# Kernel tuning notes

Hardware: AMD Instinct MI355X
Metric: run time of the kernel (lower is better)

Reference implementation:

```python
import jax, jax.numpy as jnp
import numpy as np

B, T, OBS = 256, 512, 256
H = 128          # OptimizedLSTMCell hidden size (hardcoded in module)
LATENT = 16


def setup_inputs() -> dict:
    key = jax.random.key(0)
    ks = jax.random.split(key, 6)
    xs = jax.random.normal(ks[0], (B, T, OBS), dtype=jnp.float32)
    # fused LSTM weights: gates ordered (i, f, g, o), each of width H
    Wx = jax.random.normal(ks[1], (OBS, 4 * H), dtype=jnp.float32) / np.sqrt(OBS)
    Wh = jax.random.normal(ks[2], (H, 4 * H), dtype=jnp.float32) / np.sqrt(H)
    b = jnp.zeros((4 * H,), dtype=jnp.float32)
    W1 = jax.random.normal(ks[3], (H, H), dtype=jnp.float32) / np.sqrt(H)
    b1 = jnp.zeros((H,), dtype=jnp.float32)
    W2 = jax.random.normal(ks[4], (H, 2 * LATENT), dtype=jnp.float32) / np.sqrt(H)
    b2 = jnp.zeros((2 * LATENT,), dtype=jnp.float32)
    return {"xs": xs, "Wx": Wx, "Wh": Wh, "b": b,
            "W1": W1, "b1": b1, "W2": W2, "b2": b2}


def reference(xs, Wx, Wh, b, W1, b1, W2, b2):
    # LSTM over time (flax OptimizedLSTMCell math, zero initial carry)
    bsz = xs.shape[0]
    hdim = Wh.shape[0]

    def step(carry, x_t):
        c, h = carry
        gates = x_t @ Wx + h @ Wh + b            # [B, 4H]
        i, f, g, o = jnp.split(gates, 4, axis=-1)
        i = jax.nn.sigmoid(i)
        f = jax.nn.sigmoid(f)
        g = jnp.tanh(g)
        o = jax.nn.sigmoid(o)
        c = f * c + i * g
        h = o * jnp.tanh(c)
        return (c, h), None

    init = (jnp.zeros((bsz, hdim), xs.dtype), jnp.zeros((bsz, hdim), xs.dtype))
    (_, h_last), _ = jax.lax.scan(step, init, jnp.swapaxes(xs, 0, 1))

    out = jax.nn.relu(h_last @ W1 + b1)          # [B, H]
    p = out @ W2 + b2                            # [B, 2*latent]
    mean, logvar = jnp.split(p, 2, axis=-1)
    return mean, logvar
```

## Files before the change

kernel.cpp:

```cpp
#include <hip/hip_runtime.h>
#include <hip/hip_fp16.h>

typedef unsigned short u16;
typedef unsigned int u32;

#define B_   256
#define T_   512
#define OBS_ 256
#define H_   128
#define G4_  512
#define LAT_ 16

typedef _Float16 half8_t __attribute__((ext_vector_type(8)));
typedef _Float16 half2_t __attribute__((ext_vector_type(2)));
typedef float    f32x4_t __attribute__((ext_vector_type(4)));

#if defined(__has_builtin)
#if __has_builtin(__builtin_amdgcn_fdot2)
#define HAVE_FDOT2 1
#endif
#endif

__device__ __forceinline__ u16 f2h(float x) { return __half_as_ushort(__float2half(x)); }
__device__ __forceinline__ float h2f(u16 u) { return __half2float(__ushort_as_half(u)); }
__device__ __forceinline__ float frcp(float x) { return __builtin_amdgcn_rcpf(x); }
__device__ __forceinline__ float fsigmoid(float x) { return frcp(1.f + __expf(-x)); }
__device__ __forceinline__ float ftanh(float x) { return 1.f - 2.f * frcp(1.f + __expf(2.f * x)); }

__device__ __forceinline__ float dot2acc(u32 w, u32 h, float acc) {
  half2_t wv = __builtin_bit_cast(half2_t, w);
  half2_t hv = __builtin_bit_cast(half2_t, h);
#ifdef HAVE_FDOT2
  return __builtin_amdgcn_fdot2(wv, hv, acc, false);
#else
  acc = fmaf((float)wv.x, (float)hv.x, acc);
  acc = fmaf((float)wv.y, (float)hv.y, acc);
  return acc;
#endif
}

__global__ __launch_bounds__(256) void prep_kernel(const float* __restrict__ Wx,
                                                   const float* __restrict__ Wh,
                                                   u16* __restrict__ Wxt,
                                                   u32* __restrict__ Whp) {
  int idx = blockIdx.x * 256 + threadIdx.x;
  if (idx < G4_ * OBS_) {
    int n = idx / OBS_, k = idx % OBS_;
    Wxt[idx] = f2h(Wx[(size_t)k * G4_ + n]);
  } else {
    int i2 = idx - G4_ * OBS_;
    if (i2 < (H_ / 2) * G4_) {
      int k2 = i2 / G4_, j = i2 % G4_;
      u32 lo = f2h(Wh[(size_t)(2 * k2) * G4_ + j]);
      u32 hi = f2h(Wh[(size_t)(2 * k2 + 1) * G4_ + j]);
      Whp[i2] = lo | (hi << 16);
    }
  }
}

__global__ __launch_bounds__(256, 2) void gemm_xw(const float* __restrict__ xs,
                                                  const u16* __restrict__ Wxt,
                                                  u16* __restrict__ Xw,
                                                  int t0, int ct_log2) {
  __shared__ __align__(16) u16 As[128][88];
  __shared__ __align__(16) u16 Bs[128][88];

  const int tid  = threadIdx.x;
  const int lane = tid & 63;
  const int w    = tid >> 6;
  const int qr   = (w & 1) * 64;
  const int qc   = (w >> 1) * 64;
  const int bn   = blockIdx.x;
  const int bm   = blockIdx.y;

  f32x4_t acc[4][4];
#pragma unroll
  for (int a = 0; a < 4; ++a)
#pragma unroll
    for (int bq = 0; bq < 4; ++bq)
      acc[a][bq] = (f32x4_t){0.f, 0.f, 0.f, 0.f};

  const int row  = tid >> 1;
  const int half = (tid & 1) * 32;
  const int m    = bm * 128 + row;
  const int bb   = m >> ct_log2;
  const int tau  = m & ((1 << ct_log2) - 1);
  const float* asrc = xs + (size_t)(bb * T_ + t0 + tau) * OBS_ + half;
  const u16*   bsrc = Wxt + (size_t)(bn * 128 + row) * OBS_ + half;

  for (int k0 = 0; k0 < OBS_; k0 += 64) {
    {
      const float* s = asrc + k0;
#pragma unroll
      for (int i = 0; i < 4; ++i) {
        float4 v0 = *(const float4*)(s + i * 8);
        float4 v1 = *(const float4*)(s + i * 8 + 4);
        uint4 pk;
        pk.x = (u32)f2h(v0.x) | ((u32)f2h(v0.y) << 16);
        pk.y = (u32)f2h(v0.z) | ((u32)f2h(v0.w) << 16);
        pk.z = (u32)f2h(v1.x) | ((u32)f2h(v1.y) << 16);
        pk.w = (u32)f2h(v1.z) | ((u32)f2h(v1.w) << 16);
        *(uint4*)&As[row][half + i * 8] = pk;
      }
    }
    {
      const u16* s = bsrc + k0;
#pragma unroll
      for (int i = 0; i < 4; ++i)
        *(uint4*)&Bs[row][half + i * 8] = *(const uint4*)(s + i * 8);
    }
    __syncthreads();
#pragma unroll
    for (int ks = 0; ks < 2; ++ks) {
      const int kc = ks * 32 + (lane >> 4) * 8;
      half8_t af[4], bf[4];
#pragma unroll
      for (int mi = 0; mi < 4; ++mi) af[mi] = *(const half8_t*)&As[qr + mi * 16 + (lane & 15)][kc];
#pragma unroll
      for (int ni = 0; ni < 4; ++ni) bf[ni] = *(const half8_t*)&Bs[qc + ni * 16 + (lane & 15)][kc];
#pragma unroll
      for (int mi = 0; mi < 4; ++mi)
#pragma unroll
        for (int ni = 0; ni < 4; ++ni)
          acc[mi][ni] = __builtin_amdgcn_mfma_f32_16x16x32_f16(af[mi], bf[ni], acc[mi][ni], 0, 0, 0);
    }
    __syncthreads();
  }
#pragma unroll
  for (int mi = 0; mi < 4; ++mi)
#pragma unroll
    for (int ni = 0; ni < 4; ++ni)
#pragma unroll
      for (int r = 0; r < 4; ++r) {
        int mm = bm * 128 + qr + mi * 16 + (lane >> 4) * 4 + r;
        int nn = bn * 128 + qc + ni * 16 + (lane & 15);
        Xw[(size_t)mm * G4_ + nn] = f2h(acc[mi][ni][r]);
      }
}

__global__ __launch_bounds__(512, 1) void lstm_rec(const u16* __restrict__ Xw,
                                                   const u32* __restrict__ Whp,
                                                   const float* __restrict__ bias,
                                                   float* __restrict__ c_ws,
                                                   u16* __restrict__ h_ws,
                                                   int t0, int CT) {
  const int bb = blockIdx.x;
  const int j  = threadIdx.x;
  __shared__ uint4 hq[16];
  __shared__ float g[512];

  u32 wh[64];
#pragma unroll
  for (int k2 = 0; k2 < 64; ++k2) wh[k2] = Whp[k2 * 512 + j];
  const float bj = bias[j];

  float c = 0.f;
  if (t0 == 0) {
    if (j < 16) hq[j] = make_uint4(0u, 0u, 0u, 0u);
  } else {
    if (j < 128) {
      ((u16*)hq)[j] = h_ws[bb * 128 + j];
      c = c_ws[bb * 128 + j];
    }
  }
  __syncthreads();

  const u16* xwp = Xw + (size_t)bb * CT * 512 + j;
  float xw_cur = h2f(xwp[0]);
  for (int t = 0; t < CT; ++t) {
    int tn = (t + 1 < CT) ? t + 1 : t;
    float xw_nxt = h2f(xwp[(size_t)tn * 512]);

    float a0 = 0.f, a1 = 0.f, a2 = 0.f, a3 = 0.f;
#pragma unroll
    for (int q = 0; q < 16; ++q) {
      uint4 hv = hq[q];
      a0 = dot2acc(wh[4 * q + 0], hv.x, a0);
      a1 = dot2acc(wh[4 * q + 1], hv.y, a1);
      a2 = dot2acc(wh[4 * q + 2], hv.z, a2);
      a3 = dot2acc(wh[4 * q + 3], hv.w, a3);
    }
    g[j] = ((a0 + a1) + (a2 + a3)) + bj + xw_cur;
    __syncthreads();
    if (j < 128) {
      float pi = g[j], pf = g[j + 128], pg = g[j + 256], po = g[j + 384];
      float ig = fsigmoid(pi);
      float fg = fsigmoid(pf);
      float gg = ftanh(pg);
      float og = fsigmoid(po);
      c = fg * c + ig * gg;
      float h = og * ftanh(c);
      ((u16*)hq)[j] = f2h(h);
    }
    __syncthreads();
    xw_cur = xw_nxt;
  }
  if (j < 128) {
    c_ws[bb * 128 + j] = c;
    h_ws[bb * 128 + j] = ((u16*)hq)[j];
  }
}

__global__ __launch_bounds__(128) void head_kernel(const u16* __restrict__ h_ws,
                                                   const float* __restrict__ W1,
                                                   const float* __restrict__ b1,
                                                   const float* __restrict__ W2,
                                                   const float* __restrict__ b2,
                                                   float* __restrict__ out) {
  const int bb = blockIdx.x;
  const int j  = threadIdx.x;
  __shared__ float hs[128];
  __shared__ float o1[128];
  hs[j] = h2f(h_ws[bb * 128 + j]);
  __syncthreads();
  float acc = b1[j];
#pragma unroll 8
  for (int k = 0; k < 128; ++k) acc = fmaf(hs[k], W1[(size_t)k * 128 + j], acc);
  o1[j] = fmaxf(acc, 0.f);
  __syncthreads();
  if (j < 2 * LAT_) {
    float acc2 = b2[j];
#pragma unroll 8
    for (int k = 0; k < 128; ++k) acc2 = fmaf(o1[k], W2[(size_t)k * (2 * LAT_) + j], acc2);
    if (j < LAT_) out[(size_t)bb * LAT_ + j] = acc2;
    else          out[(size_t)B_ * LAT_ + (size_t)bb * LAT_ + (j - LAT_)] = acc2;
  }
}

extern "C" void kernel_launch(void* const* d_in, const int* in_sizes, int n_in,
                              void* d_out, int out_size, void* d_ws, size_t ws_size,
                              hipStream_t stream) {
  const float* xs   = (const float*)d_in[0];
  const float* Wx   = (const float*)d_in[1];
  const float* Wh   = (const float*)d_in[2];
  const float* bias = (const float*)d_in[3];
  const float* W1   = (const float*)d_in[4];
  const float* b1   = (const float*)d_in[5];
  const float* W2   = (const float*)d_in[6];
  const float* b2   = (const float*)d_in[7];
  float* out = (float*)d_out;

  char* ws = (char*)d_ws;
  u16* Wxt  = (u16*)(ws + 0);
  u32* Whp  = (u32*)(ws + 262144);
  float* c_ws = (float*)(ws + 393216);
  u16* h_ws   = (u16*)(ws + 524288);
  u16* Xw     = (u16*)(ws + 589824);

  int CT = 512;
  while (CT > 128 && 589824 + (size_t)262144 * CT > ws_size) CT >>= 1;
  int ctl = __builtin_ctz((unsigned)CT);

  prep_kernel<<<640, 256, 0, stream>>>(Wx, Wh, Wxt, Whp);
  for (int t0 = 0; t0 < T_; t0 += CT) {
    gemm_xw<<<dim3(4, 2 * CT), 256, 0, stream>>>(xs, Wxt, Xw, t0, ctl);
    lstm_rec<<<256, 512, 0, stream>>>(Xw, Whp, bias, c_ws, h_ws, t0, CT);
  }
  head_kernel<<<256, 128, 0, stream>>>(h_ws, W1, b1, W2, b2, out);
}
```

Before: 440.7 us.

## Interleave gate columns so LSTM step uses shuffles and one barrier

Permutes the gate columns of Wx, Wh and the bias so that each hidden unit's four gates sit in adjacent lanes. The recurrent kernel then gathers gates with cross-lane shuffles instead of a shared-memory gate buffer, and double-buffers h so each timestep needs one barrier instead of two. The time loop is unrolled by four, with Xw prefetched four steps ahead. This cuts per-step synchronisation and LDS traffic on the serial critical path, but only a quarter of the lanes now do the nonlinearity work.

```diff
diff --git a/kernel.cpp b/kernel.cpp
--- a/kernel.cpp
+++ b/kernel.cpp
@@ -39,22 +39,28 @@
 #endif
 }
 
+__device__ __forceinline__ int permcol(int n) { return (n & 3) * 128 + (n >> 2); }
+
 __global__ __launch_bounds__(256) void prep_kernel(const float* __restrict__ Wx,
                                                    const float* __restrict__ Wh,
+                                                   const float* __restrict__ bias,
                                                    u16* __restrict__ Wxt,
-                                                   u32* __restrict__ Whp) {
+                                                   u32* __restrict__ Whp,
+                                                   float* __restrict__ biasp) {
   int idx = blockIdx.x * 256 + threadIdx.x;
   if (idx < G4_ * OBS_) {
     int n = idx / OBS_, k = idx % OBS_;
-    Wxt[idx] = f2h(Wx[(size_t)k * G4_ + n]);
-  } else {
+    Wxt[idx] = f2h(Wx[(size_t)k * G4_ + permcol(n)]);
+  } else if (idx < G4_ * OBS_ + (H_ / 2) * G4_) {
     int i2 = idx - G4_ * OBS_;
-    if (i2 < (H_ / 2) * G4_) {
-      int k2 = i2 / G4_, j = i2 % G4_;
-      u32 lo = f2h(Wh[(size_t)(2 * k2) * G4_ + j]);
-      u32 hi = f2h(Wh[(size_t)(2 * k2 + 1) * G4_ + j]);
-      Whp[i2] = lo | (hi << 16);
-    }
+    int k2 = i2 / G4_, n = i2 % G4_;
+    int pn = permcol(n);
+    u32 lo = f2h(Wh[(size_t)(2 * k2) * G4_ + pn]);
+    u32 hi = f2h(Wh[(size_t)(2 * k2 + 1) * G4_ + pn]);
+    Whp[i2] = lo | (hi << 16);
+  } else if (idx < G4_ * OBS_ + (H_ / 2) * G4_ + G4_) {
+    int n = idx - G4_ * OBS_ - (H_ / 2) * G4_;
+    biasp[n] = bias[permcol(n)];
   }
 }
 
@@ -140,64 +146,77 @@
 
 __global__ __launch_bounds__(512, 1) void lstm_rec(const u16* __restrict__ Xw,
                                                    const u32* __restrict__ Whp,
-                                                   const float* __restrict__ bias,
+                                                   const float* __restrict__ biasp,
                                                    float* __restrict__ c_ws,
                                                    u16* __restrict__ h_ws,
                                                    int t0, int CT) {
   const int bb = blockIdx.x;
-  const int j  = threadIdx.x;
-  __shared__ uint4 hq[16];
-  __shared__ float g[512];
+  const int tn = threadIdx.x;
+  const int q  = tn & 3;
+  const int j  = tn >> 2;
+  __shared__ uint4 hq[2][16];
 
   u32 wh[64];
 #pragma unroll
-  for (int k2 = 0; k2 < 64; ++k2) wh[k2] = Whp[k2 * 512 + j];
-  const float bj = bias[j];
+  for (int k2 = 0; k2 < 64; ++k2) wh[k2] = Whp[k2 * 512 + tn];
+#pragma unroll
+  for (int k2 = 0; k2 < 64; ++k2) asm volatile("" : "+v"(wh[k2]));
+  const float bj = biasp[tn];
 
   float c = 0.f;
   if (t0 == 0) {
-    if (j < 16) hq[j] = make_uint4(0u, 0u, 0u, 0u);
+    if (tn < 32) ((uint4*)hq)[tn] = make_uint4(0u, 0u, 0u, 0u);
   } else {
-    if (j < 128) {
-      ((u16*)hq)[j] = h_ws[bb * 128 + j];
-      c = c_ws[bb * 128 + j];
-    }
+    if (tn < 128) ((u16*)hq[0])[tn] = h_ws[bb * 128 + tn];
+    if (q == 0) c = c_ws[bb * 128 + j];
   }
   __syncthreads();
 
-  const u16* xwp = Xw + (size_t)bb * CT * 512 + j;
-  float xw_cur = h2f(xwp[0]);
-  for (int t = 0; t < CT; ++t) {
-    int tn = (t + 1 < CT) ? t + 1 : t;
-    float xw_nxt = h2f(xwp[(size_t)tn * 512]);
-
+  const u16* xwp = Xw + (size_t)bb * CT * 512 + tn;
+
+  auto step = [&](u16 xcur, int cur) {
     float a0 = 0.f, a1 = 0.f, a2 = 0.f, a3 = 0.f;
 #pragma unroll
-    for (int q = 0; q < 16; ++q) {
-      uint4 hv = hq[q];
-      a0 = dot2acc(wh[4 * q + 0], hv.x, a0);
-      a1 = dot2acc(wh[4 * q + 1], hv.y, a1);
-      a2 = dot2acc(wh[4 * q + 2], hv.z, a2);
-      a3 = dot2acc(wh[4 * q + 3], hv.w, a3);
-    }
-    g[j] = ((a0 + a1) + (a2 + a3)) + bj + xw_cur;
+    for (int qq = 0; qq < 16; ++qq) {
+      uint4 hv = hq[cur][qq];
+      a0 = dot2acc(wh[4 * qq + 0], hv.x, a0);
+      a1 = dot2acc(wh[4 * qq + 1], hv.y, a1);
+      a2 = dot2acc(wh[4 * qq + 2], hv.z, a2);
+      a3 = dot2acc(wh[4 * qq + 3], hv.w, a3);
+    }
+    float pre = ((a0 + a1) + (a2 + a3)) + bj + h2f(xcur);
+    float s1 = __shfl_xor(pre, 1);
+    float s2 = __shfl_xor(pre, 2);
+    float s3 = __shfl_xor(s1, 2);
+    if (q == 0) {
+      float ig = fsigmoid(pre);
+      float fg = fsigmoid(s1);
+      float gg = ftanh(s2);
+      float og = fsigmoid(s3);
+      c = fg * c + ig * gg;
+      ((u16*)hq[cur ^ 1])[j] = f2h(og * ftanh(c));
+    }
     __syncthreads();
-    if (j < 128) {
-      float pi = g[j], pf = g[j + 128], pg = g[j + 256], po = g[j + 384];
-      float ig = fsigmoid(pi);
-      float fg = fsigmoid(pf);
-      float gg = ftanh(pg);
-      float og = fsigmoid(po);
-      c = fg * c + ig * gg;
-      float h = og * ftanh(c);
-      ((u16*)hq)[j] = f2h(h);
-    }
-    __syncthreads();
-    xw_cur = xw_nxt;
-  }
-  if (j < 128) {
+  };
+
+  u16 x0 = xwp[0 * 512], x1 = xwp[1 * 512], x2 = xwp[2 * 512], x3 = xwp[3 * 512];
+  for (int t = 0; t < CT; t += 4) {
+    u16 n0 = 0, n1 = 0, n2 = 0, n3 = 0;
+    if (t + 4 < CT) {
+      n0 = xwp[(size_t)(t + 4) * 512];
+      n1 = xwp[(size_t)(t + 5) * 512];
+      n2 = xwp[(size_t)(t + 6) * 512];
+      n3 = xwp[(size_t)(t + 7) * 512];
+    }
+    step(x0, 0);
+    step(x1, 1);
+    step(x2, 0);
+    step(x3, 1);
+    x0 = n0; x1 = n1; x2 = n2; x3 = n3;
+  }
+  if (q == 0) {
     c_ws[bb * 128 + j] = c;
-    h_ws[bb * 128 + j] = ((u16*)hq)[j];
+    h_ws[bb * 128 + j] = ((u16*)hq[0])[j];
   }
 }
 
@@ -241,20 +260,21 @@
   float* out = (float*)d_out;
 
   char* ws = (char*)d_ws;
-  u16* Wxt  = (u16*)(ws + 0);
-  u32* Whp  = (u32*)(ws + 262144);
+  u16* Wxt    = (u16*)(ws + 0);
+  u32* Whp    = (u32*)(ws + 262144);
   float* c_ws = (float*)(ws + 393216);
   u16* h_ws   = (u16*)(ws + 524288);
-  u16* Xw     = (u16*)(ws + 589824);
+  float* biasp= (float*)(ws + 589824);
+  u16* Xw     = (u16*)(ws + 591872);
 
   int CT = 512;
-  while (CT > 128 && 589824 + (size_t)262144 * CT > ws_size) CT >>= 1;
+  while (CT > 128 && 591872 + (size_t)262144 * CT > ws_size) CT >>= 1;
   int ctl = __builtin_ctz((unsigned)CT);
 
-  prep_kernel<<<640, 256, 0, stream>>>(Wx, Wh, Wxt, Whp);
+  prep_kernel<<<642, 256, 0, stream>>>(Wx, Wh, bias, Wxt, Whp, biasp);
   for (int t0 = 0; t0 < T_; t0 += CT) {
     gemm_xw<<<dim3(4, 2 * CT), 256, 0, stream>>>(xs, Wxt, Xw, t0, ctl);
-    lstm_rec<<<256, 512, 0, stream>>>(Xw, Whp, bias, c_ws, h_ws, t0, CT);
+    lstm_rec<<<256, 512, 0, stream>>>(Xw, Whp, biasp, c_ws, h_ws, t0, CT);
   }
   head_kernel<<<256, 128, 0, stream>>>(h_ws, W1, b1, W2, b2, out);
 }
```

Measured after the change: 441.5 us. Within noise of the previous version (+0.2%).

## Run LSTM recurrence on MFMA with 16-batch tiles and permuted gate layout

Applied to the files above, without the earlier changes.

Replaces the per-batch dot2 recurrence kernel (256 blocks, one batch row each) with an MFMA-based kernel in which each block handles 16 batch rows. Wh is kept in registers as MFMA A-fragments, and h is double-buffered in LDS, which leaves one barrier per step instead of two. Gate columns are permuted so that each lane's accumulator holds i, f, g and o for the same hidden unit, so the nonlinearities run in registers without an LDS round-trip. The bias is folded into the input-projection GEMM, and Xw rows are prefetched four steps ahead. The trade-off is that only 16 blocks run, using far fewer CUs, so the gain relies on lower per-step latency rather than parallelism.

```diff
diff --git a/kernel.cpp b/kernel.cpp
--- a/kernel.cpp
+++ b/kernel.cpp
@@ -15,51 +15,43 @@
 typedef _Float16 half2_t __attribute__((ext_vector_type(2)));
 typedef float    f32x4_t __attribute__((ext_vector_type(4)));
 
-#if defined(__has_builtin)
-#if __has_builtin(__builtin_amdgcn_fdot2)
-#define HAVE_FDOT2 1
-#endif
-#endif
-
 __device__ __forceinline__ u16 f2h(float x) { return __half_as_ushort(__float2half(x)); }
 __device__ __forceinline__ float h2f(u16 u) { return __half2float(__ushort_as_half(u)); }
 __device__ __forceinline__ float frcp(float x) { return __builtin_amdgcn_rcpf(x); }
 __device__ __forceinline__ float fsigmoid(float x) { return frcp(1.f + __expf(-x)); }
 __device__ __forceinline__ float ftanh(float x) { return 1.f - 2.f * frcp(1.f + __expf(2.f * x)); }
 
-__device__ __forceinline__ float dot2acc(u32 w, u32 h, float acc) {
-  half2_t wv = __builtin_bit_cast(half2_t, w);
-  half2_t hv = __builtin_bit_cast(half2_t, h);
-#ifdef HAVE_FDOT2
-  return __builtin_amdgcn_fdot2(wv, hv, acc, false);
-#else
-  acc = fmaf((float)wv.x, (float)hv.x, acc);
-  acc = fmaf((float)wv.y, (float)hv.y, acc);
-  return acc;
-#endif
-}
+__device__ __forceinline__ int sigma_c(int s) {
+  return (s & 3) * 128 + (s >> 6) * 16 + ((s >> 2) & 3) * 4 + ((s >> 4) & 3);
+}
+__device__ __forceinline__ int perm_g(int g) { return (g & 3) * 128 + (g >> 2); }
 
 __global__ __launch_bounds__(256) void prep_kernel(const float* __restrict__ Wx,
                                                    const float* __restrict__ Wh,
+                                                   const float* __restrict__ bias,
                                                    u16* __restrict__ Wxt,
-                                                   u32* __restrict__ Whp) {
+                                                   u32* __restrict__ WhA,
+                                                   float* __restrict__ biasp) {
   int idx = blockIdx.x * 256 + threadIdx.x;
   if (idx < G4_ * OBS_) {
-    int n = idx / OBS_, k = idx % OBS_;
-    Wxt[idx] = f2h(Wx[(size_t)k * G4_ + n]);
-  } else {
+    int s = idx / OBS_, k = idx % OBS_;
+    Wxt[idx] = f2h(Wx[(size_t)k * G4_ + sigma_c(s)]);
+  } else if (idx < G4_ * OBS_ + 64 * G4_) {
     int i2 = idx - G4_ * OBS_;
-    if (i2 < (H_ / 2) * G4_) {
-      int k2 = i2 / G4_, j = i2 % G4_;
-      u32 lo = f2h(Wh[(size_t)(2 * k2) * G4_ + j]);
-      u32 hi = f2h(Wh[(size_t)(2 * k2 + 1) * G4_ + j]);
-      Whp[i2] = lo | (hi << 16);
-    }
+    int g = i2 >> 6, k2 = i2 & 63;
+    int pg = perm_g(g);
+    u32 lo = f2h(Wh[(size_t)(2 * k2) * G4_ + pg]);
+    u32 hi = f2h(Wh[(size_t)(2 * k2 + 1) * G4_ + pg]);
+    WhA[(size_t)g * 64 + k2] = lo | (hi << 16);
+  } else if (idx < G4_ * OBS_ + 64 * G4_ + G4_) {
+    int s = idx - G4_ * OBS_ - 64 * G4_;
+    biasp[s] = bias[sigma_c(s)];
   }
 }
 
 __global__ __launch_bounds__(256, 2) void gemm_xw(const float* __restrict__ xs,
                                                   const u16* __restrict__ Wxt,
+                                                  const float* __restrict__ biasp,
                                                   u16* __restrict__ Xw,
                                                   int t0, int ct_log2) {
   __shared__ __align__(16) u16 As[128][88];
@@ -75,10 +67,12 @@
 
   f32x4_t acc[4][4];
 #pragma unroll
-  for (int a = 0; a < 4; ++a)
-#pragma unroll
-    for (int bq = 0; bq < 4; ++bq)
-      acc[a][bq] = (f32x4_t){0.f, 0.f, 0.f, 0.f};
+  for (int ni = 0; ni < 4; ++ni) {
+    float b = biasp[bn * 128 + qc + ni * 16 + (lane & 15)];
+#pragma unroll
+    for (int mi = 0; mi < 4; ++mi)
+      acc[mi][ni] = (f32x4_t){b, b, b, b};
+  }
 
   const int row  = tid >> 1;
   const int half = (tid & 1) * 32;
@@ -90,11 +84,11 @@
 
   for (int k0 = 0; k0 < OBS_; k0 += 64) {
     {
-      const float* s = asrc + k0;
+      const float* sp = asrc + k0;
 #pragma unroll
       for (int i = 0; i < 4; ++i) {
-        float4 v0 = *(const float4*)(s + i * 8);
-        float4 v1 = *(const float4*)(s + i * 8 + 4);
+        float4 v0 = *(const float4*)(sp + i * 8);
+        float4 v1 = *(const float4*)(sp + i * 8 + 4);
         uint4 pk;
         pk.x = (u32)f2h(v0.x) | ((u32)f2h(v0.y) << 16);
         pk.y = (u32)f2h(v0.z) | ((u32)f2h(v0.w) << 16);
@@ -104,10 +98,10 @@
       }
     }
     {
-      const u16* s = bsrc + k0;
+      const u16* sp = bsrc + k0;
 #pragma unroll
       for (int i = 0; i < 4; ++i)
-        *(uint4*)&Bs[row][half + i * 8] = *(const uint4*)(s + i * 8);
+        *(uint4*)&Bs[row][half + i * 8] = *(const uint4*)(sp + i * 8);
     }
     __syncthreads();
 #pragma unroll
@@ -138,66 +132,117 @@
       }
 }
 
-__global__ __launch_bounds__(512, 1) void lstm_rec(const u16* __restrict__ Xw,
-                                                   const u32* __restrict__ Whp,
-                                                   const float* __restrict__ bias,
-                                                   float* __restrict__ c_ws,
-                                                   u16* __restrict__ h_ws,
-                                                   int t0, int CT) {
-  const int bb = blockIdx.x;
-  const int j  = threadIdx.x;
-  __shared__ uint4 hq[16];
-  __shared__ float g[512];
-
-  u32 wh[64];
-#pragma unroll
-  for (int k2 = 0; k2 < 64; ++k2) wh[k2] = Whp[k2 * 512 + j];
-  const float bj = bias[j];
-
-  float c = 0.f;
-  if (t0 == 0) {
-    if (j < 16) hq[j] = make_uint4(0u, 0u, 0u, 0u);
-  } else {
-    if (j < 128) {
-      ((u16*)hq)[j] = h_ws[bb * 128 + j];
-      c = c_ws[bb * 128 + j];
+#define HLS2 72
+
+__global__ __launch_bounds__(512, 2)
+void lstm_mfma(const u16* __restrict__ Xw,
+               const u32* __restrict__ WhA,
+               float* __restrict__ c_ws,
+               u16* __restrict__ h_ws,
+               int t0, int CT) {
+  const int tid  = threadIdx.x;
+  const int lane = tid & 63;
+  const int wave = tid >> 6;
+  const int n    = lane & 15;
+  const int kg   = lane >> 4;
+  const int b0   = blockIdx.x * 16;
+
+  __shared__ u32 hl[2][16 * HLS2];
+
+  uint4 A[4][4];
+#pragma unroll
+  for (int ti = 0; ti < 4; ++ti) {
+    const int mg = (wave * 4 + ti) * 16 + n;
+    const u32* ap = WhA + (size_t)mg * 64 + kg * 4;
+#pragma unroll
+    for (int kf = 0; kf < 4; ++kf)
+      asm volatile("global_load_dwordx4 %0, %1, off" : "=v"(A[ti][kf]) : "v"(ap + kf * 16));
+  }
+  asm volatile("s_waitcnt vmcnt(0)" ::: "memory");
+  __builtin_amdgcn_sched_barrier(0);
+
+  float c_reg[4], h_last[4];
+#pragma unroll
+  for (int ti = 0; ti < 4; ++ti) { c_reg[ti] = 0.f; h_last[ti] = 0.f; }
+  if (t0 != 0) {
+#pragma unroll
+    for (int ti = 0; ti < 4; ++ti)
+      c_reg[ti] = c_ws[(size_t)(b0 + n) * 128 + (wave * 4 + ti) * 4 + kg];
+  }
+  {
+    const u32* hws32 = (const u32*)h_ws;
+    for (int idx = tid; idx < 16 * 64; idx += 512) {
+      int r = idx >> 6, k2 = idx & 63;
+      hl[0][r * HLS2 + k2] = (t0 == 0) ? 0u : hws32[(size_t)(b0 + r) * 64 + k2];
     }
   }
   __syncthreads();
 
-  const u16* xwp = Xw + (size_t)bb * CT * 512 + j;
-  float xw_cur = h2f(xwp[0]);
-  for (int t = 0; t < CT; ++t) {
-    int tn = (t + 1 < CT) ? t + 1 : t;
-    float xw_nxt = h2f(xwp[(size_t)tn * 512]);
-
-    float a0 = 0.f, a1 = 0.f, a2 = 0.f, a3 = 0.f;
-#pragma unroll
-    for (int q = 0; q < 16; ++q) {
-      uint4 hv = hq[q];
-      a0 = dot2acc(wh[4 * q + 0], hv.x, a0);
-      a1 = dot2acc(wh[4 * q + 1], hv.y, a1);
-      a2 = dot2acc(wh[4 * q + 2], hv.z, a2);
-      a3 = dot2acc(wh[4 * q + 3], hv.w, a3);
-    }
-    g[j] = ((a0 + a1) + (a2 + a3)) + bj + xw_cur;
+  const u16* xrow = Xw + (size_t)((b0 + n) * CT) * 512 + wave * 64 + kg * 16;
+
+  auto step = [&](const uint4& va, const uint4& vb, int cur) {
+    const u32* hb = hl[cur];
+    uint4 Bf[4];
+#pragma unroll
+    for (int kf = 0; kf < 4; ++kf)
+      Bf[kf] = *(const uint4*)&hb[n * HLS2 + kf * 16 + kg * 4];
+    u32 xv[8] = {va.x, va.y, va.z, va.w, vb.x, vb.y, vb.z, vb.w};
+#pragma unroll
+    for (int ti = 0; ti < 4; ++ti) {
+      f32x4_t acc = (f32x4_t){0.f, 0.f, 0.f, 0.f};
+#pragma unroll
+      for (int kf = 0; kf < 4; ++kf)
+        acc = __builtin_amdgcn_mfma_f32_16x16x32_f16(
+            __builtin_bit_cast(half8_t, A[ti][kf]),
+            __builtin_bit_cast(half8_t, Bf[kf]), acc, 0, 0, 0);
+      half2_t xlo = __builtin_bit_cast(half2_t, xv[2 * ti]);
+      half2_t xhi = __builtin_bit_cast(half2_t, xv[2 * ti + 1]);
+      float ig = fsigmoid(acc[0] + (float)xlo[0]);
+      float fg = fsigmoid(acc[1] + (float)xlo[1]);
+      float gt = ftanh   (acc[2] + (float)xhi[0]);
+      float og = fsigmoid(acc[3] + (float)xhi[1]);
+      c_reg[ti] = fmaf(fg, c_reg[ti], ig * gt);
+      float h = og * ftanh(c_reg[ti]);
+      h_last[ti] = h;
+      const int j = (wave * 4 + ti) * 4 + kg;
+      ((u16*)&hl[cur ^ 1][0])[(n * HLS2 + (j >> 1)) * 2 + (j & 1)] = f2h(h);
+    }
     __syncthreads();
-    if (j < 128) {
-      float pi = g[j], pf = g[j + 128], pg = g[j + 256], po = g[j + 384];
-      float ig = fsigmoid(pi);
-      float fg = fsigmoid(pf);
-      float gg = ftanh(pg);
-      float og = fsigmoid(po);
-      c = fg * c + ig * gg;
-      float h = og * ftanh(c);
-      ((u16*)hq)[j] = f2h(h);
-    }
-    __syncthreads();
-    xw_cur = xw_nxt;
-  }
-  if (j < 128) {
-    c_ws[bb * 128 + j] = c;
-    h_ws[bb * 128 + j] = ((u16*)hq)[j];
+  };
+
+  uint4 q0a = *(const uint4*)(xrow + 0 * 512);
+  uint4 q0b = *(const uint4*)(xrow + 0 * 512 + 8);
+  uint4 q1a = *(const uint4*)(xrow + 1 * 512);
+  uint4 q1b = *(const uint4*)(xrow + 1 * 512 + 8);
+  uint4 q2a = *(const uint4*)(xrow + 2 * 512);
+  uint4 q2b = *(const uint4*)(xrow + 2 * 512 + 8);
+  uint4 q3a = *(const uint4*)(xrow + 3 * 512);
+  uint4 q3b = *(const uint4*)(xrow + 3 * 512 + 8);
+
+  for (int base = 0; base < CT; base += 4) {
+    int r0 = base + 4 < CT ? base + 4 : CT - 1;
+    int r1 = base + 5 < CT ? base + 5 : CT - 1;
+    int r2 = base + 6 < CT ? base + 6 : CT - 1;
+    int r3 = base + 7 < CT ? base + 7 : CT - 1;
+    step(q0a, q0b, 0);
+    q0a = *(const uint4*)(xrow + (size_t)r0 * 512);
+    q0b = *(const uint4*)(xrow + (size_t)r0 * 512 + 8);
+    step(q1a, q1b, 1);
+    q1a = *(const uint4*)(xrow + (size_t)r1 * 512);
+    q1b = *(const uint4*)(xrow + (size_t)r1 * 512 + 8);
+    step(q2a, q2b, 0);
+    q2a = *(const uint4*)(xrow + (size_t)r2 * 512);
+    q2b = *(const uint4*)(xrow + (size_t)r2 * 512 + 8);
+    step(q3a, q3b, 1);
+    q3a = *(const uint4*)(xrow + (size_t)r3 * 512);
+    q3b = *(const uint4*)(xrow + (size_t)r3 * 512 + 8);
+  }
+
+#pragma unroll
+  for (int ti = 0; ti < 4; ++ti) {
+    const int j = (wave * 4 + ti) * 4 + kg;
+    c_ws[(size_t)(b0 + n) * 128 + j] = c_reg[ti];
+    h_ws[(size_t)(b0 + n) * 128 + j] = f2h(h_last[ti]);
   }
 }
 
@@ -241,20 +286,21 @@
   float* out = (float*)d_out;
 
   char* ws = (char*)d_ws;
-  u16* Wxt  = (u16*)(ws + 0);
-  u32* Whp  = (u32*)(ws + 262144);
+  u16* Wxt    = (u16*)(ws + 0);
+  u32* WhA    = (u32*)(ws + 262144);
   float* c_ws = (float*)(ws + 393216);
   u16* h_ws   = (u16*)(ws + 524288);
-  u16* Xw     = (u16*)(ws + 589824);
+  float* biasp= (float*)(ws + 589824);
+  u16* Xw     = (u16*)(ws + 591872);
 
   int CT = 512;
-  while (CT > 128 && 589824 + (size_t)262144 * CT > ws_size) CT >>= 1;
+  while (CT > 128 && 591872 + (size_t)262144 * CT > ws_size) CT >>= 1;
   int ctl = __builtin_ctz((unsigned)CT);
 
-  prep_kernel<<<640, 256, 0, stream>>>(Wx, Wh, Wxt, Whp);
+  prep_kernel<<<642, 256, 0, stream>>>(Wx, Wh, bias, Wxt, WhA, biasp);
   for (int t0 = 0; t0 < T_; t0 += CT) {
-    gemm_xw<<<dim3(4, 2 * CT), 256, 0, stream>>>(xs, Wxt, Xw, t0, ctl);
-    lstm_rec<<<256, 512, 0, stream>>>(Xw, Whp, bias, c_ws, h_ws, t0, CT);
+    gemm_xw<<<dim3(4, 2 * CT), 256, 0, stream>>>(xs, Wxt, biasp, Xw, t0, ctl);
+    lstm_mfma<<<16, 512, 0, stream>>>(Xw, WhA, c_ws, h_ws, t0, CT);
   }
   head_kernel<<<256, 128, 0, stream>>>(h_ws, W1, b1, W2, b2, out);
 }
```

New measurement: 723.7 us. +64.2%, slower.
